# Optimization experiments

Measured on AMD Instinct MI355X. Metric: run time of the kernel, lower is better.

The kernel has to match this reference:

```python
import jax, jax.numpy as jnp
import numpy as np

B, T, I, H, BU = 64, 512, 256, 512, 1024  # batch, seq, input, hidden, backbone_units


def _lecun(x):
    return 1.7159 * jnp.tanh(0.666 * x)


def setup_inputs() -> dict:
    key = jax.random.key(0)
    ks = jax.random.split(key, 13)
    s = 0.03  # small init to keep gates unsaturated
    return {
        "x": jax.random.normal(ks[0], (B, T, I), jnp.float32),
        "wb1": jax.random.normal(ks[1], (BU, I + H), jnp.float32) * s,
        "bb1": jnp.zeros((BU,), jnp.float32),
        "wb2": jax.random.normal(ks[2], (BU, BU), jnp.float32) * s,
        "bb2": jnp.zeros((BU,), jnp.float32),
        "wff1": jax.random.normal(ks[3], (H, BU), jnp.float32) * s,
        "bff1": jnp.zeros((H,), jnp.float32),
        "wff2": jax.random.normal(ks[4], (H, BU), jnp.float32) * s,
        "bff2": jnp.zeros((H,), jnp.float32),
        "wta": jax.random.normal(ks[5], (H, BU), jnp.float32) * s,
        "bta": jnp.zeros((H,), jnp.float32),
        "wtb": jax.random.normal(ks[6], (H, BU), jnp.float32) * s,
        "btb": jnp.zeros((H,), jnp.float32),
    }


def reference(x, wb1, bb1, wb2, bb2, wff1, bff1, wff2, bff2, wta, bta, wtb, btb):
    ts = jnp.float32(1.0)  # timespans=None -> ts = 1.0 each step

    def step(h, xt):
        z = jnp.concatenate([xt, h], axis=-1)            # [B, I+H]
        z = _lecun(z @ wb1.T + bb1)                      # backbone layer 1
        z = _lecun(z @ wb2.T + bb2)                      # backbone layer 2
        ff1 = jnp.tanh(z @ wff1.T + bff1)
        ff2 = jnp.tanh(z @ wff2.T + bff2)
        t_a = z @ wta.T + bta
        t_b = z @ wtb.T + btb
        t_interp = jax.nn.sigmoid(t_a * ts + t_b)
        h_new = ff1 * (1.0 - t_interp) + t_interp * ff2  # default mode
        return h_new, h_new

    h0 = jnp.zeros((x.shape[0], wff1.shape[0]), x.dtype)
    xs = jnp.swapaxes(x, 0, 1)                           # [T, B, I]
    _, ys = jax.lax.scan(step, h0, xs)                   # ys: [T, B, H]
    return jnp.swapaxes(ys, 0, 1)                        # [B, T, H]
```

## Files before the change

kernel.cpp:

```cpp
#include <hip/hip_runtime.h>
#include <hip/hip_bf16.h>


#define Tt  512
#define Ii  256
#define Hh  512
#define BUu 1024

typedef __attribute__((ext_vector_type(8))) short bf16x8;
typedef __attribute__((ext_vector_type(4))) float f32x4;

#define OFF_WB1   0u
#define OFF_WB2   1572864u
#define OFF_WHD   3670016u
#define OFF_Z1    6815744u
#define OFF_Z2    6946816u
#define OFF_H     7077888u
#define OFF_FLAGS 7143424u
#define OFF_POOL  7147520u

#define SM_WB1 0
#define SM_WB2 49152
#define SM_SA  114688
#define SM_XA  118784
#define SM_TOTAL 120832

__device__ __forceinline__ short f2bf(float f) {
  unsigned u = __builtin_bit_cast(unsigned, f);
  u += 0x7FFFu + ((u >> 16) & 1u);
  return (short)(u >> 16);
}
__device__ __forceinline__ float fast_tanh(float u) {
  float e = __expf(2.0f * u);
  return (e - 1.0f) / (e + 1.0f);
}
__device__ __forceinline__ float fast_sig(float x) {
  return 1.0f / (1.0f + __expf(-x));
}
__device__ __forceinline__ float lecun_act(float u) {
  return 1.7159f * fast_tanh(0.666f * u);
}

__device__ __forceinline__ void burst8(const void* p, bf16x8* v) {
  asm volatile(
      "global_load_dwordx4 %0, %8, off sc0\n\t"
      "global_load_dwordx4 %1, %8, off offset:64 sc0\n\t"
      "global_load_dwordx4 %2, %8, off offset:128 sc0\n\t"
      "global_load_dwordx4 %3, %8, off offset:192 sc0\n\t"
      "global_load_dwordx4 %4, %8, off offset:256 sc0\n\t"
      "global_load_dwordx4 %5, %8, off offset:320 sc0\n\t"
      "global_load_dwordx4 %6, %8, off offset:384 sc0\n\t"
      "global_load_dwordx4 %7, %8, off offset:448 sc0\n\t"
      "s_waitcnt vmcnt(0)"
      : "=&v"(v[0]), "=&v"(v[1]), "=&v"(v[2]), "=&v"(v[3]),
        "=&v"(v[4]), "=&v"(v[5]), "=&v"(v[6]), "=&v"(v[7])
      : "v"(p));
}
__device__ __forceinline__ void burst16(const void* p, bf16x8* v) {
  asm volatile(
      "global_load_dwordx4 %0, %16, off sc0\n\t"
      "global_load_dwordx4 %1, %16, off offset:64 sc0\n\t"
      "global_load_dwordx4 %2, %16, off offset:128 sc0\n\t"
      "global_load_dwordx4 %3, %16, off offset:192 sc0\n\t"
      "global_load_dwordx4 %4, %16, off offset:256 sc0\n\t"
      "global_load_dwordx4 %5, %16, off offset:320 sc0\n\t"
      "global_load_dwordx4 %6, %16, off offset:384 sc0\n\t"
      "global_load_dwordx4 %7, %16, off offset:448 sc0\n\t"
      "global_load_dwordx4 %8, %16, off offset:512 sc0\n\t"
      "global_load_dwordx4 %9, %16, off offset:576 sc0\n\t"
      "global_load_dwordx4 %10, %16, off offset:640 sc0\n\t"
      "global_load_dwordx4 %11, %16, off offset:704 sc0\n\t"
      "global_load_dwordx4 %12, %16, off offset:768 sc0\n\t"
      "global_load_dwordx4 %13, %16, off offset:832 sc0\n\t"
      "global_load_dwordx4 %14, %16, off offset:896 sc0\n\t"
      "global_load_dwordx4 %15, %16, off offset:960 sc0\n\t"
      "s_waitcnt vmcnt(0)"
      : "=&v"(v[0]), "=&v"(v[1]), "=&v"(v[2]), "=&v"(v[3]),
        "=&v"(v[4]), "=&v"(v[5]), "=&v"(v[6]), "=&v"(v[7]),
        "=&v"(v[8]), "=&v"(v[9]), "=&v"(v[10]), "=&v"(v[11]),
        "=&v"(v[12]), "=&v"(v[13]), "=&v"(v[14]), "=&v"(v[15])
      : "v"(p));
}
__device__ __forceinline__ unsigned apoll(unsigned* p) {
  unsigned old;
  asm volatile("global_atomic_add %0, %1, %2, off sc0\n\ts_waitcnt vmcnt(0)"
               : "=&v"(old) : "v"(p), "v"(0u) : "memory");
  return old;
}
__device__ __forceinline__ void inv_l1() {
  asm volatile("buffer_inv sc0\n\ts_waitcnt vmcnt(0)" ::: "memory");
}

__device__ __forceinline__ void bar_arrive(unsigned* cnt, int tid) {
  __syncthreads();
  if (tid == 0)
    asm volatile("global_atomic_add %0, %1, off" :: "v"(cnt), "v"(1u) : "memory");
}
__device__ __forceinline__ void bar_wait(unsigned* cnt, int tid, unsigned target,
                                         volatile unsigned* eph) {
  if (tid == 0) {
    for (int spin = 0; spin < (1 << 15); ++spin) {
      if (apoll(cnt) >= target) break;
      __builtin_amdgcn_s_sleep(1);
    }
    *eph = target;
  }
  while (*eph < target) __builtin_amdgcn_s_sleep(1);
  inv_l1();
}

__global__ void cfc_prep(const float* __restrict__ wb1, const float* __restrict__ wb2,
                         const float* __restrict__ wff1, const float* __restrict__ wff2,
                         const float* __restrict__ wta, const float* __restrict__ wtb,
                         unsigned char* __restrict__ ws) {
  const unsigned N1 = 1024u * 768u;
  const unsigned N2 = 1024u * 1024u;
  const unsigned N3 = 1536u * 1024u;
  const unsigned NH = 32768u;
  const unsigned NF = 1040u;
  unsigned idx = blockIdx.x * blockDim.x + threadIdx.x;
  short* Wb1 = (short*)(ws + OFF_WB1);
  short* Wb2 = (short*)(ws + OFF_WB2);
  short* Whd = (short*)(ws + OFF_WHD);
  short* Hbuf = (short*)(ws + OFF_H);
  unsigned* flags = (unsigned*)(ws + OFF_FLAGS);
  if (idx < N1) { Wb1[idx] = f2bf(wb1[idx]); return; }
  idx -= N1;
  if (idx < N2) { Wb2[idx] = f2bf(wb2[idx]); return; }
  idx -= N2;
  if (idx < N3) {
    unsigned c = idx >> 10, k = idx & 1023u;
    unsigned i = c / 3u, hd = c % 3u;
    float v = (hd == 0u) ? wff1[i * 1024u + k]
            : (hd == 1u) ? wff2[i * 1024u + k]
                         : (wta[i * 1024u + k] + wtb[i * 1024u + k]);
    Whd[idx] = f2bf(v);
    return;
  }
  idx -= N3;
  if (idx < NH) { Hbuf[idx] = 0; return; }
  idx -= NH;
  if (idx < NF) { flags[idx] = 0u; }
}

__global__ __launch_bounds__(256, 1) void cfc_run(
    const float* __restrict__ x,
    const float* __restrict__ bb1, const float* __restrict__ bb2,
    const float* __restrict__ bff1, const float* __restrict__ bff2,
    const float* __restrict__ bta, const float* __restrict__ btb,
    unsigned char* __restrict__ ws, float* __restrict__ out) {
  extern __shared__ char smem[];
  __shared__ int sh_rank;
  __shared__ volatile unsigned sh_epoch;
  const int tid = threadIdx.x;
  const int w = tid >> 6;
  const int lane = tid & 63;

  unsigned xcc;
  asm volatile("s_getreg_b32 %0, hwreg(HW_REG_XCC_ID)" : "=s"(xcc));
  xcc &= 7u;
  unsigned* pools = (unsigned*)(ws + OFF_POOL);
  if (tid == 0) {
    sh_rank = (int)atomicAdd(pools + xcc, 1u);
    sh_epoch = 0u;
  }
  __syncthreads();
  const int r = sh_rank & 31;

  const short* Wb1 = (const short*)(ws + OFF_WB1);
  const short* Wb2 = (const short*)(ws + OFF_WB2);
  const short* Whd = (const short*)(ws + OFF_WHD);
  char* z1_x = (char*)(ws + OFF_Z1) + (xcc << 14);
  char* z2_x = (char*)(ws + OFF_Z2) + (xcc << 14);
  char* h_x  = (char*)(ws + OFF_H)  + (xcc << 13);
  unsigned* cnt = (unsigned*)(ws + OFF_FLAGS + (xcc << 9));

  const int m0 = (int)xcc << 3;
  const int n0 = r << 5;
  const int ib = r << 4;

  const int row16 = lane & 15;
  const int row8 = row16 & 7;
  const int kg = lane >> 4;
  const int kg16 = kg << 4;
  const int swzm = (row16 & 7) << 4;
  const int tw = w >> 1, hw = w & 1;

  for (int c = tid; c < 32 * 96; c += 256) {
    int rr = c / 96, kb = (c % 96) << 4;
    *(bf16x8*)(smem + SM_WB1 + rr * 1536 + (kb ^ ((rr & 7) << 4))) =
        *(const bf16x8*)(Wb1 + (size_t)(n0 + rr) * 768 + (kb >> 1));
  }
  for (int c = tid; c < 32 * 128; c += 256) {
    int rr = c >> 7, kb = (c & 127) << 4;
    *(bf16x8*)(smem + SM_WB2 + rr * 2048 + (kb ^ ((rr & 7) << 4))) =
        *(const bf16x8*)(Wb2 + (size_t)(n0 + rr) * 1024 + (kb >> 1));
  }

  bf16x8 whd[32];
  if (w < 3) {
    const short* wp = Whd + (size_t)(r * 48 + w * 16 + row16) * 1024 + kg * 8;
#pragma unroll
    for (int kc = 0; kc < 32; ++kc) whd[kc] = *(const bf16x8*)(wp + kc * 32);
  }

  float* SAf = (float*)(smem + SM_SA);
  float* XAf = (float*)(smem + SM_XA);

  const int et = tid >> 7, err = (tid >> 4) & 7, ecc = tid & 15;
  const int elane = ((err >> 2) << 4) + ecc, ei = err & 3;
  const float b1e = bb1[n0 + et * 16 + ecc];
  const float b2e = bb2[n0 + et * 16 + ecc];
  const int rr3 = tid >> 4, il3 = tid & 15;
  float bf1e = 0.f, bf2e = 0.f, btabe = 0.f;
  if (tid < 128) {
    bf1e = bff1[ib + il3];
    bf2e = bff2[ib + il3];
    btabe = bta[ib + il3] + btb[ib + il3];
  }

  auto xpart = [&](int tn) {
    const float* xr = x + (size_t)(m0 + row8) * (Tt * Ii) + (size_t)tn * Ii;
    bf16x8 a[8];
#pragma unroll
    for (int kc = 0; kc < 8; ++kc) {
      const f32x4 va = *(const f32x4*)(xr + kc * 32 + kg * 8);
      const f32x4 vb = *(const f32x4*)(xr + kc * 32 + kg * 8 + 4);
#pragma unroll
      for (int j = 0; j < 4; ++j) { a[kc][j] = f2bf(va[j]); a[kc][4 + j] = f2bf(vb[j]); }
    }
    f32x4 q00 = {0.f,0.f,0.f,0.f}, q01 = {0.f,0.f,0.f,0.f};
    f32x4 q10 = {0.f,0.f,0.f,0.f}, q11 = {0.f,0.f,0.f,0.f};
#pragma unroll
    for (int kc = 0; kc < 8; ++kc) {
      const bf16x8 b0 = *(const bf16x8*)(smem + SM_WB1 + row16 * 1536 + (((kc << 6) + kg16) ^ swzm));
      const bf16x8 b1 = *(const bf16x8*)(smem + SM_WB1 + (16 + row16) * 1536 + (((kc << 6) + kg16) ^ swzm));
      if (kc & 1) {
        q01 = __builtin_amdgcn_mfma_f32_16x16x32_bf16(a[kc], b0, q01, 0, 0, 0);
        q11 = __builtin_amdgcn_mfma_f32_16x16x32_bf16(a[kc], b1, q11, 0, 0, 0);
      } else {
        q00 = __builtin_amdgcn_mfma_f32_16x16x32_bf16(a[kc], b0, q00, 0, 0, 0);
        q10 = __builtin_amdgcn_mfma_f32_16x16x32_bf16(a[kc], b1, q10, 0, 0, 0);
      }
    }
    *(f32x4*)(XAf + 0 * 256 + lane * 4) = q00 + q01;
    *(f32x4*)(XAf + 1 * 256 + lane * 4) = q10 + q11;
  };

  __syncthreads();
  if (w == 3) xpart(0);
  __syncthreads();

#pragma unroll 1
  for (int t = 0; t < Tt; ++t) {
    const unsigned g1 = 3u * t + 1u, g2 = 3u * t + 2u, g3 = 3u * t + 3u;
    if (t) bar_wait(cnt, tid, 32u * (3u * t), &sh_epoch);

    {
      f32x4 acc0, acc1 = {0.f,0.f,0.f,0.f};
      if (hw == 0) acc0 = *(const f32x4*)(XAf + tw * 256 + lane * 4);
      else         acc0 = f32x4{0.f,0.f,0.f,0.f};
      bf16x8 ha[8];
      burst8(h_x + (row8 << 10) + (kg << 4) + (hw << 9), ha);
#pragma unroll
      for (int k = 0; k < 8; ++k) {
        const int kc = 8 + hw * 8 + k;
        const bf16x8 b = *(const bf16x8*)(smem + SM_WB1 + (tw * 16 + row16) * 1536 + (((kc << 6) + kg16) ^ swzm));
        if (k & 1) acc1 = __builtin_amdgcn_mfma_f32_16x16x32_bf16(ha[k], b, acc1, 0, 0, 0);
        else       acc0 = __builtin_amdgcn_mfma_f32_16x16x32_bf16(ha[k], b, acc0, 0, 0, 0);
      }
      const f32x4 asum = acc0 + acc1;
      *(f32x4*)(SAf + (tw * 2 + hw) * 256 + lane * 4) = asum;
      __syncthreads();
      const float v = SAf[(et * 2 + 0) * 256 + elane * 4 + ei] +
                      SAf[(et * 2 + 1) * 256 + elane * 4 + ei] + b1e;
      *(short*)(z1_x + err * 2048 + ((n0 + et * 16 + ecc) << 1)) = f2bf(lecun_act(v));
    }
    bar_arrive(cnt, tid);
    bar_wait(cnt, tid, 32u * g1, &sh_epoch);

    {
      bf16x8 zb[16];
      burst16(z1_x + (row8 << 11) + (kg << 4) + (hw << 10), zb);
      f32x4 acc0 = {0.f,0.f,0.f,0.f}, acc1 = {0.f,0.f,0.f,0.f};
#pragma unroll
      for (int k = 0; k < 16; ++k) {
        const int kc = hw * 16 + k;
        const bf16x8 b = *(const bf16x8*)(smem + SM_WB2 + (tw * 16 + row16) * 2048 + (((kc << 6) + kg16) ^ swzm));
        if (k & 1) acc1 = __builtin_amdgcn_mfma_f32_16x16x32_bf16(zb[k], b, acc1, 0, 0, 0);
        else       acc0 = __builtin_amdgcn_mfma_f32_16x16x32_bf16(zb[k], b, acc0, 0, 0, 0);
      }
      const f32x4 asum = acc0 + acc1;
      __syncthreads();
      *(f32x4*)(SAf + (tw * 2 + hw) * 256 + lane * 4) = asum;
      __syncthreads();
      const float v = SAf[(et * 2 + 0) * 256 + elane * 4 + ei] +
                      SAf[(et * 2 + 1) * 256 + elane * 4 + ei] + b2e;
      *(short*)(z2_x + err * 2048 + ((n0 + et * 16 + ecc) << 1)) = f2bf(lecun_act(v));
    }
    bar_arrive(cnt, tid);

    if (w < 3) {
      bar_wait(cnt, tid, 32u * g2, &sh_epoch);
      f32x4 p0 = {0.f,0.f,0.f,0.f}, p1 = {0.f,0.f,0.f,0.f};
      bf16x8 za[16];
      burst16(z2_x + (row8 << 11) + (kg << 4), za);
#pragma unroll
      for (int k = 0; k < 16; ++k) {
        if (k & 1) p1 = __builtin_amdgcn_mfma_f32_16x16x32_bf16(za[k], whd[k], p1, 0, 0, 0);
        else       p0 = __builtin_amdgcn_mfma_f32_16x16x32_bf16(za[k], whd[k], p0, 0, 0, 0);
      }
      burst16(z2_x + (row8 << 11) + (kg << 4) + 1024, za);
#pragma unroll
      for (int k = 0; k < 16; ++k) {
        if (k & 1) p1 = __builtin_amdgcn_mfma_f32_16x16x32_bf16(za[k], whd[16 + k], p1, 0, 0, 0);
        else       p0 = __builtin_amdgcn_mfma_f32_16x16x32_bf16(za[k], whd[16 + k], p0, 0, 0, 0);
      }
      *(f32x4*)(SAf + w * 256 + lane * 4) = p0 + p1;
    } else {
      if (t + 1 < Tt) xpart(t + 1);
    }
    __syncthreads();
    if (tid < 128) {
      float d[3];
#pragma unroll
      for (int hd = 0; hd < 3; ++hd) {
        const int hc = 3 * il3 + hd;
        d[hd] = SAf[(hc >> 4) * 256 + ((((rr3 >> 2) << 4) + (hc & 15)) << 2) + (rr3 & 3)];
      }
      const float ff1 = fast_tanh(d[0] + bf1e);
      const float ff2 = fast_tanh(d[1] + bf2e);
      const float tt  = fast_sig(d[2] + btabe);
      const float hn = ff1 + tt * (ff2 - ff1);
      *(short*)(h_x + (rr3 << 10) + ((ib + il3) << 1)) = f2bf(hn);
      out[(size_t)(m0 + rr3) * (Tt * Hh) + (size_t)t * Hh + ib + il3] = hn;
    }
    bar_arrive(cnt, tid);
  }
}

extern "C" void kernel_launch(void* const* d_in, const int* in_sizes, int n_in,
                              void* d_out, int out_size, void* d_ws, size_t ws_size,
                              hipStream_t stream) {
  const float* x    = (const float*)d_in[0];
  const float* wb1  = (const float*)d_in[1];
  const float* bb1  = (const float*)d_in[2];
  const float* wb2  = (const float*)d_in[3];
  const float* bb2  = (const float*)d_in[4];
  const float* wff1 = (const float*)d_in[5];
  const float* bff1 = (const float*)d_in[6];
  const float* wff2 = (const float*)d_in[7];
  const float* bff2 = (const float*)d_in[8];
  const float* wta  = (const float*)d_in[9];
  const float* bta  = (const float*)d_in[10];
  const float* wtb  = (const float*)d_in[11];
  const float* btb  = (const float*)d_in[12];
  unsigned char* ws = (unsigned char*)d_ws;

  const unsigned prep_items = 786432u + 1048576u + 1572864u + 32768u + 1040u;
  cfc_prep<<<(prep_items + 255u) / 256u, 256, 0, stream>>>(wb1, wb2, wff1, wff2, wta, wtb, ws);
  cfc_run<<<256, 256, SM_TOTAL, stream>>>(x, bb1, bb2, bff1, bff2, bta, btb, ws, (float*)d_out);
}
```

Measured before the change: 6.448 ms.

## Replace atomic-counter grid barrier with per-block flags and master release

```diff
diff --git a/kernel.cpp b/kernel.cpp
--- a/kernel.cpp
+++ b/kernel.cpp
@@ -17,7 +17,7 @@
 #define OFF_Z2    6946816u
 #define OFF_H     7077888u
 #define OFF_FLAGS 7143424u
-#define OFF_POOL  7147520u
+#define OFF_POOL  7176192u
 
 #define SM_WB1 0
 #define SM_WB2 49152
@@ -87,25 +87,37 @@
                : "=&v"(old) : "v"(p), "v"(0u) : "memory");
   return old;
 }
+__device__ __forceinline__ void aswap(unsigned* p, unsigned v) {
+  asm volatile("global_atomic_swap %0, %1, off" :: "v"(p), "v"(v) : "memory");
+}
 __device__ __forceinline__ void inv_l1() {
   asm volatile("buffer_inv sc0\n\ts_waitcnt vmcnt(0)" ::: "memory");
 }
 
-__device__ __forceinline__ void bar_arrive(unsigned* cnt, int tid) {
+__device__ __forceinline__ void bar_arrive(unsigned* arr, int r, int tid, unsigned g) {
   __syncthreads();
-  if (tid == 0)
-    asm volatile("global_atomic_add %0, %1, off" :: "v"(cnt), "v"(1u) : "memory");
-}
-__device__ __forceinline__ void bar_wait(unsigned* cnt, int tid, unsigned target,
+  if (tid == 0) aswap(arr + r * 16, g);
+}
+__device__ __forceinline__ void bar_wait(unsigned* arr, unsigned* rel, int r,
+                                         int w, int lane, int tid, unsigned g,
                                          volatile unsigned* eph) {
-  if (tid == 0) {
+  if (r == 0 && w == 0) {
+    unsigned* ap = arr + (lane & 31) * 16;
     for (int spin = 0; spin < (1 << 15); ++spin) {
-      if (apoll(cnt) >= target) break;
+      unsigned f = apoll(ap);
+      if (__all((int)(f >= g))) break;
       __builtin_amdgcn_s_sleep(1);
     }
-    *eph = target;
-  }
-  while (*eph < target) __builtin_amdgcn_s_sleep(1);
+    if (lane < 32) aswap(rel + lane * 16, g);
+    if (lane == 0) *eph = g;
+  } else if (tid == 0) {
+    for (int spin = 0; spin < (1 << 15); ++spin) {
+      if (apoll(rel + r * 16) >= g) break;
+      __builtin_amdgcn_s_sleep(1);
+    }
+    *eph = g;
+  }
+  while (*eph < g) __builtin_amdgcn_s_sleep(1);
   inv_l1();
 }
 
@@ -117,7 +129,7 @@
   const unsigned N2 = 1024u * 1024u;
   const unsigned N3 = 1536u * 1024u;
   const unsigned NH = 32768u;
-  const unsigned NF = 1040u;
+  const unsigned NF = 8208u;
   unsigned idx = blockIdx.x * blockDim.x + threadIdx.x;
   short* Wb1 = (short*)(ws + OFF_WB1);
   short* Wb2 = (short*)(ws + OFF_WB2);
@@ -173,7 +185,8 @@
   char* z1_x = (char*)(ws + OFF_Z1) + (xcc << 14);
   char* z2_x = (char*)(ws + OFF_Z2) + (xcc << 14);
   char* h_x  = (char*)(ws + OFF_H)  + (xcc << 13);
-  unsigned* cnt = (unsigned*)(ws + OFF_FLAGS + (xcc << 9));
+  unsigned* arr = (unsigned*)(ws + OFF_FLAGS + (xcc << 12));
+  unsigned* rel = (unsigned*)(ws + OFF_FLAGS + (xcc << 12) + 2048);
 
   const int m0 = (int)xcc << 3;
   const int n0 = r << 5;
@@ -254,7 +267,7 @@
 #pragma unroll 1
   for (int t = 0; t < Tt; ++t) {
     const unsigned g1 = 3u * t + 1u, g2 = 3u * t + 2u, g3 = 3u * t + 3u;
-    if (t) bar_wait(cnt, tid, 32u * (3u * t), &sh_epoch);
+    if (t) bar_wait(arr, rel, r, w, lane, tid, 3u * t, &sh_epoch);
 
     {
       f32x4 acc0, acc1 = {0.f,0.f,0.f,0.f};
@@ -276,8 +289,8 @@
                       SAf[(et * 2 + 1) * 256 + elane * 4 + ei] + b1e;
       *(short*)(z1_x + err * 2048 + ((n0 + et * 16 + ecc) << 1)) = f2bf(lecun_act(v));
     }
-    bar_arrive(cnt, tid);
-    bar_wait(cnt, tid, 32u * g1, &sh_epoch);
+    bar_arrive(arr, r, tid, g1);
+    bar_wait(arr, rel, r, w, lane, tid, g1, &sh_epoch);
 
     {
       bf16x8 zb[16];
@@ -298,10 +311,10 @@
                       SAf[(et * 2 + 1) * 256 + elane * 4 + ei] + b2e;
       *(short*)(z2_x + err * 2048 + ((n0 + et * 16 + ecc) << 1)) = f2bf(lecun_act(v));
     }
-    bar_arrive(cnt, tid);
+    bar_arrive(arr, r, tid, g2);
 
     if (w < 3) {
-      bar_wait(cnt, tid, 32u * g2, &sh_epoch);
+      bar_wait(arr, rel, r, w, lane, tid, g2, &sh_epoch);
       f32x4 p0 = {0.f,0.f,0.f,0.f}, p1 = {0.f,0.f,0.f,0.f};
       bf16x8 za[16];
       burst16(z2_x + (row8 << 11) + (kg << 4), za);
@@ -335,7 +348,7 @@
       *(short*)(h_x + (rr3 << 10) + ((ib + il3) << 1)) = f2bf(hn);
       out[(size_t)(m0 + rr3) * (Tt * Hh) + (size_t)t * Hh + ib + il3] = hn;
     }
-    bar_arrive(cnt, tid);
+    bar_arrive(arr, r, tid, g3);
   }
 }
 
@@ -357,7 +370,7 @@
   const float* btb  = (const float*)d_in[12];
   unsigned char* ws = (unsigned char*)d_ws;
 
-  const unsigned prep_items = 786432u + 1048576u + 1572864u + 32768u + 1040u;
+  const unsigned prep_items = 786432u + 1048576u + 1572864u + 32768u + 8208u;
   cfc_prep<<<(prep_items + 255u) / 256u, 256, 0, stream>>>(wb1, wb2, wff1, wff2, wta, wtb, ws);
   cfc_run<<<256, 256, SM_TOTAL, stream>>>(x, bb1, bb2, bff1, bff2, bta, btb, ws, (float*)d_out);
 }
```

Result: slower. 6.810 ms (+5.6%).
